# Kernel optimization log

Measured on AMD Instinct MI355X. Metric: run time of the kernel, lower is better.

## Reference

```python
import jax, jax.numpy as jnp
import numpy as np

N, E, IN, H, L = 50000, 640000, 64, 128, 3
EPS_DIST = 1e-8
LN_EPS = 1e-5


def setup_inputs() -> dict:
    key = jax.random.key(0)
    ks = iter(jax.random.split(key, 64))

    def rn(shape, fan_in):
        return (jax.random.normal(next(ks), shape, jnp.float32) / np.sqrt(fan_in)).astype(jnp.float32)

    inp = {}
    inp['h'] = jax.random.normal(next(ks), (N, IN), jnp.float32)
    inp['x'] = jax.random.normal(next(ks), (N, 3), jnp.float32)
    inp['edge_index'] = jax.random.randint(next(ks), (2, E), 0, N, jnp.int64)
    # embedding_in: Linear(IN, H)
    inp['W_emb'] = rn((IN, H), IN); inp['b_emb'] = jnp.zeros((H,), jnp.float32)
    # per-layer EquivariantConv params, stacked over L
    inp['Wm1'] = rn((L, 2 * H + 1, H), 2 * H + 1); inp['bm1'] = jnp.zeros((L, H), jnp.float32)
    inp['Wm2'] = rn((L, H, H), H);                 inp['bm2'] = jnp.zeros((L, H), jnp.float32)
    inp['Wc1'] = rn((L, H, H), H);                 inp['bc1'] = jnp.zeros((L, H), jnp.float32)
    inp['Wc2'] = rn((L, H, 1), H)  # no bias
    inp['Wn1'] = rn((L, 2 * H, H), 2 * H);         inp['bn1'] = jnp.zeros((L, H), jnp.float32)
    inp['Wn2'] = rn((L, H, H), H);                 inp['bn2'] = jnp.zeros((L, H), jnp.float32)
    inp['ln_g'] = jnp.ones((L, H), jnp.float32);   inp['ln_b'] = jnp.zeros((L, H), jnp.float32)
    # epsilon head params
    inp['Wem1'] = rn((2 * H + 4, H), 2 * H + 4);   inp['bem1'] = jnp.zeros((H,), jnp.float32)
    inp['Wem2'] = rn((H, H), H);                   inp['bem2'] = jnp.zeros((H,), jnp.float32)
    inp['Wec1'] = rn((H, H), H);                   inp['bec1'] = jnp.zeros((H,), jnp.float32)
    inp['Wec2'] = rn((H, 3), H);                   inp['bec2'] = jnp.zeros((3,), jnp.float32)
    inp['Wh1'] = rn((H + 3, H), H + 3);            inp['bh1'] = jnp.zeros((H,), jnp.float32)
    inp['Wh2'] = rn((H, 3), H);                    inp['bh2'] = jnp.zeros((3,), jnp.float32)
    return inp


def _layernorm(v, g, b):
    mu = jnp.mean(v, axis=-1, keepdims=True)
    var = jnp.mean((v - mu) ** 2, axis=-1, keepdims=True)
    return (v - mu) * jax.lax.rsqrt(var + LN_EPS) * g + b


def reference(h, x, edge_index, W_emb, b_emb, Wm1, bm1, Wm2, bm2, Wc1, bc1, Wc2,
              Wn1, bn1, Wn2, bn2, ln_g, ln_b, Wem1, bem1, Wem2, bem2,
              Wec1, bec1, Wec2, bec2, Wh1, bh1, Wh2, bh2):
    row, col = edge_index[0], edge_index[1]
    n = x.shape[0]
    seg = lambda v: jax.ops.segment_sum(v, col, num_segments=n)
    in_degree = seg(jnp.ones((col.shape[0], 1), x.dtype))  # [N,1]

    h = h @ W_emb + b_emb  # embedding_in

    for i in range(L):
        rel = x[row] - x[col]                                   # [E,3]
        dist = jnp.linalg.norm(rel, axis=-1, keepdims=True)     # [E,1]
        mi = jnp.concatenate([h[row], h[col], dist], axis=-1)   # [E,2H+1]
        m = jax.nn.silu(jax.nn.silu(mi @ Wm1[i] + bm1[i]) @ Wm2[i] + bm2[i])
        agg = seg(m)                                            # [N,H]
        rel_dir = rel / (dist + EPS_DIST)
        coord_mult = jnp.tanh(jax.nn.silu(m @ Wc1[i] + bc1[i]) @ Wc2[i])  # [E,1]
        coord_update = seg(coord_mult * rel_dir)                # [N,3]
        x = x + coord_update / (in_degree + 1.0)
        nu = jnp.concatenate([h, agg], axis=-1)
        h = h + jax.nn.silu(nu @ Wn1[i] + bn1[i]) @ Wn2[i] + bn2[i]
        h = _layernorm(h, ln_g[i], ln_b[i])

    # predict_epsilon (eps_directional_head=False, eps_use_local_head=True, eps_normalize_agg=False)
    rel = x[row] - x[col]
    dist = jnp.linalg.norm(rel, axis=-1, keepdims=True)
    mi = jnp.concatenate([h[row], h[col], rel, dist], axis=-1)  # [E,2H+4]
    em = jax.nn.silu(jax.nn.silu(mi @ Wem1 + bem1) @ Wem2 + bem2)
    eps_src = jax.nn.silu(em @ Wec1 + bec1) @ Wec2 + bec2       # [E,3]
    eps = seg(eps_src)                                          # [N,3]
    hx = jnp.concatenate([h, x], axis=-1)
    eps = eps + jax.nn.silu(hx @ Wh1 + bh1) @ Wh2 + bh2
    return (h, x, eps)
```

## Files before the change

### kernel.cpp

```cpp
#include <hip/hip_runtime.h>

#define N_NODES 50000
#define N_EDGES 640000
#define HDIM    128
#define NLAYERS 3

typedef __attribute__((ext_vector_type(4))) float f32x4;
typedef short s16x8 __attribute__((ext_vector_type(8)));
typedef __bf16 bf16v8 __attribute__((ext_vector_type(8)));

static __device__ __forceinline__ unsigned short f2b(float f){
  unsigned int u = __float_as_uint(f);
  unsigned int r = u + 0x7FFFu + ((u >> 16) & 1u);
  return (unsigned short)(r >> 16);
}
static __device__ __forceinline__ float b2f(unsigned short h){
  return __uint_as_float(((unsigned int)h) << 16);
}
static __device__ __forceinline__ float silu_f(float x){
  return x / (1.0f + __expf(-x));
}
static __device__ __forceinline__ unsigned int cvt2(float a, float b){
  unsigned int r;
  asm("v_cvt_pk_bf16_f32 %0, %1, %2" : "=v"(r) : "v"(a), "v"(b));
  return r;
}
static __device__ __forceinline__ s16x8 siluPack(const f32x4 a, const f32x4 b){
  union { unsigned int u[4]; s16x8 v; } r;
  r.u[0] = cvt2(silu_f(a[0]), silu_f(a[1]));
  r.u[1] = cvt2(silu_f(a[2]), silu_f(a[3]));
  r.u[2] = cvt2(silu_f(b[0]), silu_f(b[1]));
  r.u[3] = cvt2(silu_f(b[2]), silu_f(b[3]));
  return r.v;
}
static __device__ __forceinline__ f32x4 MFMA(s16x8 a, s16x8 b, f32x4 c){
  return __builtin_amdgcn_mfma_f32_16x16x32_bf16(
      __builtin_bit_cast(bf16v8, a), __builtin_bit_cast(bf16v8, b), c, 0, 0, 0);
}

static __device__ __forceinline__ s16x8 ldA(const unsigned short* __restrict__ WT,
                                            int K, int s, int kk, int lane){
  const unsigned short* p = WT + (size_t)((s<<4) + (lane&15))*K + (kk<<5) + ((lane>>4)<<2);
  ushort4 a = *(const ushort4*)p;
  ushort4 b = *(const ushort4*)(p + 16);
  s16x8 r;
  r[0]=(short)a.x; r[1]=(short)a.y; r[2]=(short)a.z; r[3]=(short)a.w;
  r[4]=(short)b.x; r[5]=(short)b.y; r[6]=(short)b.z; r[7]=(short)b.w;
  return r;
}
static __device__ __forceinline__ s16x8 ldBf32(const float* __restrict__ p, int q){
  float4 a = *(const float4*)(p + (q<<2));
  float4 b = *(const float4*)(p + 16 + (q<<2));
  s16x8 r;
  r[0]=(short)f2b(a.x); r[1]=(short)f2b(a.y); r[2]=(short)f2b(a.z); r[3]=(short)f2b(a.w);
  r[4]=(short)f2b(b.x); r[5]=(short)f2b(b.y); r[6]=(short)f2b(b.z); r[7]=(short)f2b(b.w);
  return r;
}

#define GLL(SRC, DST) __builtin_amdgcn_global_load_lds( \
    (const __attribute__((address_space(1))) void*)(SRC), \
    (__attribute__((address_space(3))) void*)(DST), 16, 0, 0)

struct ConvJob { const float* src; unsigned short* dst; int kshift; };
struct ConvJobs { ConvJob j[8]; };
__global__ void k_conv8(ConvJobs jobs){
  const ConvJob jb = jobs.j[blockIdx.y];
  const int K = 1 << jb.kshift;
  const int idx = (blockIdx.x<<8) + threadIdx.x;
  if (idx < (K<<7)){
    const int n = idx >> jb.kshift;
    const int k = idx & (K-1);
    jb.dst[idx] = f2b(jb.src[(size_t)k*HDIM + n]);
  }
}

struct BlobJob { const float *W1, *W2, *W3; unsigned short* dst; };
struct BlobJobs { BlobJob j[4]; };
__global__ void k_blob4(BlobJobs jobs){
  const BlobJob jb = jobs.j[blockIdx.y];
  const int i = (blockIdx.x<<8) + threadIdx.x;
  const int t = i >> 12;
  const int n = (i >> 5) & 127;
  const int slot = (i >> 3) & 3;
  const int j = i & 7;
  const int q = slot ^ ((n >> 1) & 3);
  const int kl = ((j >> 2) << 4) + (q << 2) + (j & 3);
  float v;
  if (t < 8)       v = jb.W1[(size_t)((t<<5)+kl)*HDIM + n];
  else if (t < 12) v = jb.W2[(size_t)(((t-8)<<5)+kl)*HDIM + n];
  else             v = jb.W3[(size_t)(((t-12)<<5)+kl)*HDIM + n];
  jb.dst[i] = f2b(v);
}

__global__ void k_init(const float* __restrict__ xin, float* __restrict__ xbuf,
                       float* __restrict__ cu, float* __restrict__ epsb,
                       int* __restrict__ degi){
  const int i = (blockIdx.x<<8) + threadIdx.x;
  if (i < N_NODES*3){ xbuf[i] = xin[i]; cu[i] = 0.f; epsb[i] = 0.f; }
  if (i < N_NODES) degi[i] = 0;
}

__global__ void k_degree(const int* __restrict__ coli, int* __restrict__ degi){
  const int e = (blockIdx.x<<8) + threadIdx.x;
  if (e < N_EDGES) atomicAdd(&degi[coli[e]], 1);
}
__global__ void k_scanA(const int* __restrict__ degi, int* __restrict__ off, int* __restrict__ bsum){
  const int t = threadIdx.x, b = blockIdx.x;
  const int i = (b<<8) + t;
  const int v = (i < N_NODES) ? degi[i] : 0;
  int x = v;
  const int lane = t & 63;
  #pragma unroll
  for (int d=1; d<64; d<<=1){ int y = __shfl_up(x, d); if (lane >= d) x += y; }
  __shared__ int wsum[4];
  if (lane == 63) wsum[t>>6] = x;
  __syncthreads();
  int wo = 0;
  #pragma unroll
  for (int w=0; w<4; ++w) if (w < (t>>6)) wo += wsum[w];
  const int incl = x + wo;
  if (i < N_NODES) off[i] = incl - v;
  if (t == 255) bsum[b] = incl;
}
__global__ void k_scanB(int* __restrict__ bsum, int nb){
  const int t = threadIdx.x;
  const int v = (t < nb) ? bsum[t] : 0;
  int x = v;
  const int lane = t & 63;
  #pragma unroll
  for (int d=1; d<64; d<<=1){ int y = __shfl_up(x, d); if (lane >= d) x += y; }
  __shared__ int wsum[4];
  if (lane == 63) wsum[t>>6] = x;
  __syncthreads();
  int wo = 0;
  #pragma unroll
  for (int w=0; w<4; ++w) if (w < (t>>6)) wo += wsum[w];
  const int incl = x + wo;
  if (t < nb) bsum[t] = incl - v;
}
__global__ void k_scanC(int* __restrict__ off, const int* __restrict__ bsum, int* __restrict__ cursor){
  const int i = (blockIdx.x<<8) + threadIdx.x;
  if (i < N_NODES){
    const int o = off[i] + bsum[i>>8];
    off[i] = o;
    cursor[i] = o;
  }
}
__global__ void k_fill(const int* __restrict__ coli, int* __restrict__ cursor, int* __restrict__ perm){
  const int e = (blockIdx.x<<8) + threadIdx.x;
  if (e < N_EDGES){
    const int p = atomicAdd(&cursor[coli[e]], 1);
    perm[e] = p;
  }
}

__global__ __launch_bounds__(256) void k_embed(
    const float* __restrict__ hin, const unsigned short* __restrict__ WembT,
    const float* __restrict__ bemb, float* __restrict__ hbuf,
    unsigned short* __restrict__ hb)
{
  __shared__ float s_b[128];
  const int tid = threadIdx.x;
  if (tid < 128) s_b[tid] = bemb[tid];
  __syncthreads();
  const int lane = tid & 63, q = lane>>4;
  const int n = (blockIdx.x<<6) + ((tid>>6)<<4) + (lane&15);
  const bool valid = n < N_NODES;
  const int nc = valid ? n : (N_NODES-1);
  const float* __restrict__ hp = hin + (size_t)nc*64;
  f32x4 acc[8];
  #pragma unroll
  for (int s=0;s<8;++s)
    #pragma unroll
    for (int r=0;r<4;++r) acc[s][r] = s_b[(s<<4)+(q<<2)+r];
  #pragma unroll
  for (int kk=0;kk<2;++kk){
    const s16x8 bf = ldBf32(hp + (kk<<5), q);
    #pragma unroll
    for (int s=0;s<8;++s) acc[s] = MFMA(ldA(WembT, 64, s, kk, lane), bf, acc[s]);
  }
  if (valid){
    float* op = hbuf + (size_t)n*HDIM;
    unsigned short* hbw = hb + (size_t)n*HDIM;
    #pragma unroll
    for (int s=0;s<8;++s){
      float4 o; o.x=acc[s][0]; o.y=acc[s][1]; o.z=acc[s][2]; o.w=acc[s][3];
      *(float4*)(op + (s<<4) + (q<<2)) = o;
      ushort4 u; u.x=f2b(o.x); u.y=f2b(o.y); u.z=f2b(o.z); u.w=f2b(o.w);
      *(ushort4*)(hbw + ((s>>1)<<5) + (q<<3) + ((s&1)<<2)) = u;
    }
  }
}

template<bool CSR>
__global__ __launch_bounds__(512,2) void k_edge_mlp(
    const unsigned short* __restrict__ hb, const float* __restrict__ xbuf,
    const int* __restrict__ rowi, const int* __restrict__ coli,
    const int* __restrict__ perm, const unsigned short* __restrict__ blob,
    const float* __restrict__ bm1v, const float* __restrict__ wm1r,
    const float* __restrict__ bm2v, const float* __restrict__ bc1v,
    const float* __restrict__ wc2v,
    unsigned short* __restrict__ m_buf, float* __restrict__ agg,
    float* __restrict__ cu)
{
  __shared__ struct {
    __align__(16) unsigned char wbuf[16][8192];
    int pmS[256];
    float rdS[3][256];
  } sm;
  const int tid = threadIdx.x, lane = tid & 63, q = lane >> 4;
  const int w = tid >> 6;
  const int q8 = q << 3;
  const int ebase = blockIdx.x << 8;

  #pragma unroll
  for (int t=0;t<16;++t)
    GLL(blob + (t<<12) + (tid<<3), &sm.wbuf[t][tid<<4]);

  int rn[2], cn[2];
  float dist[2];
  #pragma unroll
  for (int e=0;e<2;++e){
    const int el = (w<<5) + (e<<4) + (lane&15);
    const int ge = ebase + el;
    rn[e] = rowi[ge]; cn[e] = coli[ge];
    const float dx = xbuf[3*rn[e]+0] - xbuf[3*cn[e]+0];
    const float dy = xbuf[3*rn[e]+1] - xbuf[3*cn[e]+1];
    const float dz = xbuf[3*rn[e]+2] - xbuf[3*cn[e]+2];
    const float d = sqrtf(dx*dx + dy*dy + dz*dz);
    dist[e] = d;
    if (q == 0){
      const float inv = 1.0f / (d + 1e-8f);
      sm.rdS[0][el] = dx*inv; sm.rdS[1][el] = dy*inv; sm.rdS[2][el] = dz*inv;
      if (CSR) sm.pmS[el] = perm[ge];
    }
  }

  f32x4 acc[2][8];
  #pragma unroll
  for (int s=0;s<8;++s){
    const f32x4 b1 = *(const f32x4*)&bm1v[(s<<4)+(q<<2)];
    const f32x4 wv = *(const f32x4*)&wm1r[(s<<4)+(q<<2)];
    #pragma unroll
    for (int e=0;e<2;++e)
      #pragma unroll
      for (int r=0;r<4;++r) acc[e][s][r] = b1[r] + dist[e]*wv[r];
  }
  const int toff = ((lane&15)<<6) + ((q ^ ((lane>>1)&3))<<4);

  s16x8 B0[2], B1[2];
  #pragma unroll
  for (int e=0;e<2;++e){
    B0[e] = *(const s16x8*)(hb + ((size_t)rn[e]<<7) + q8);
    B1[e] = *(const s16x8*)(hb + ((size_t)rn[e]<<7) + 32 + q8);
  }

  __syncthreads();

  #pragma unroll
  for (int kk=0;kk<8;++kk){
    s16x8 Bn[2];
    if (kk < 6){
      const int k2 = kk+2;
      #pragma unroll
      for (int e=0;e<2;++e){
        const int node = (k2 < 4) ? rn[e] : cn[e];
        Bn[e] = *(const s16x8*)(hb + ((size_t)node<<7) + ((k2&3)<<5) + q8);
      }
    }
    #pragma unroll
    for (int s=0;s<8;++s){
      const s16x8 A = *(const s16x8*)&sm.wbuf[kk][(s<<10)+toff];
      #pragma unroll
      for (int e=0;e<2;++e) acc[e][s] = MFMA(A, B0[e], acc[e][s]);
    }
    #pragma unroll
    for (int e=0;e<2;++e){ B0[e] = B1[e]; if (kk < 6) B1[e] = Bn[e]; }
  }

  s16x8 sb[2][4];
  #pragma unroll
  for (int e=0;e<2;++e)
    #pragma unroll
    for (int c=0;c<4;++c) sb[e][c] = siluPack(acc[e][2*c], acc[e][2*c+1]);

  f32x4 acc2[2][8];
  #pragma unroll
  for (int s=0;s<8;++s){
    const f32x4 b = *(const f32x4*)&bm2v[(s<<4)+(q<<2)];
    #pragma unroll
    for (int e=0;e<2;++e) acc2[e][s] = b;
  }
  #pragma unroll
  for (int c=0;c<4;++c)
    #pragma unroll
    for (int s=0;s<8;++s){
      const s16x8 A = *(const s16x8*)&sm.wbuf[8+c][(s<<10)+toff];
      #pragma unroll
      for (int e=0;e<2;++e) acc2[e][s] = MFMA(A, sb[e][c], acc2[e][s]);
    }

  s16x8 mb[2][4];
  #pragma unroll
  for (int e=0;e<2;++e)
    #pragma unroll
    for (int c=0;c<4;++c) mb[e][c] = siluPack(acc2[e][2*c], acc2[e][2*c+1]);

  f32x4 acc3[2][8];
  #pragma unroll
  for (int s=0;s<8;++s){
    const f32x4 b = *(const f32x4*)&bc1v[(s<<4)+(q<<2)];
    #pragma unroll
    for (int e=0;e<2;++e) acc3[e][s] = b;
  }
  #pragma unroll
  for (int c=0;c<4;++c)
    #pragma unroll
    for (int s=0;s<8;++s){
      const s16x8 A = *(const s16x8*)&sm.wbuf[12+c][(s<<10)+toff];
      #pragma unroll
      for (int e=0;e<2;++e) acc3[e][s] = MFMA(A, mb[e][c], acc3[e][s]);
    }

  float dot[2] = {0.f,0.f};
  #pragma unroll
  for (int s=0;s<8;++s){
    const f32x4 wv = *(const f32x4*)&wc2v[(s<<4)+(q<<2)];
    #pragma unroll
    for (int e=0;e<2;++e)
      #pragma unroll
      for (int r=0;r<4;++r) dot[e] += silu_f(acc3[e][s][r]) * wv[r];
  }
  #pragma unroll
  for (int e=0;e<2;++e){
    dot[e] += __shfl_xor(dot[e], 16);
    dot[e] += __shfl_xor(dot[e], 32);
    const float cm = tanhf(dot[e]);
    const int el = (w<<5) + (e<<4) + (lane&15);
    if (q < 3)
      atomicAdd(&cu[(size_t)cn[e]*3 + q], cm * sm.rdS[q][el]);
  }
  if (CSR){
    #pragma unroll
    for (int e=0;e<2;++e){
      const int el = (w<<5) + (e<<4) + (lane&15);
      unsigned short* mp = m_buf + ((size_t)sm.pmS[el]<<7) + q8;
      #pragma unroll
      for (int c=0;c<4;++c) *(s16x8*)(mp + (c<<5)) = mb[e][c];
    }
  } else {
    #pragma unroll
    for (int e=0;e<2;++e){
      float* ap = agg + (size_t)cn[e]*HDIM + (q<<2);
      #pragma unroll
      for (int c=0;c<4;++c)
        #pragma unroll
        for (int j=0;j<8;++j){
          const int o = (((c<<1)+(j>>2))<<4) + (j&3);
          atomicAdd(ap + o, b2f((unsigned short)mb[e][c][j]));
        }
    }
  }
}

template<bool CSR>
__global__ __launch_bounds__(256) void k_node_mlp(
    float* __restrict__ hbuf, unsigned short* __restrict__ hb,
    float* __restrict__ xbuf,
    const unsigned short* __restrict__ m_buf, const float* __restrict__ agg,
    const int* __restrict__ off, const int* __restrict__ degi,
    float* __restrict__ cu,
    const unsigned short* __restrict__ Wn1T, const float* __restrict__ bn1v,
    const unsigned short* __restrict__ Wn2T, const float* __restrict__ bn2v,
    const float* __restrict__ lng, const float* __restrict__ lnb)
{
  __shared__ float s_bn1[128], s_bn2[128], s_g[128], s_b[128];
  const int tid = threadIdx.x;
  const int nbase = blockIdx.x << 6;
  if (tid >= 128){
    const int f = tid - 128;
    s_bn1[f]=bn1v[f]; s_bn2[f]=bn2v[f]; s_g[f]=lng[f]; s_b[f]=lnb[f];
  } else if (tid < 64){
    const int n = nbase + tid;
    if (n < N_NODES){
      const float dd = (float)degi[n] + 1.0f;
      #pragma unroll
      for (int c=0;c<3;++c){
        xbuf[3*n+c] += cu[3*n+c] / dd;
        cu[3*n+c] = 0.f;
      }
    }
  }
  __syncthreads();

  const int lane = tid & 63, q = lane >> 4;
  const int q8 = q << 3;
  const int n = nbase + ((tid>>6)<<4) + (lane & 15);
  const bool valid = (n < N_NODES);
  const int nc = valid ? n : (N_NODES-1);
  const float* __restrict__ hp = hbuf + (size_t)nc*HDIM;
  const unsigned short* __restrict__ hbp = hb + (size_t)nc*HDIM;

  float aggv[4][8];
  #pragma unroll
  for (int kk=0;kk<4;++kk)
    #pragma unroll
    for (int j=0;j<8;++j) aggv[kk][j]=0.f;
  if (CSR){
    const int st = off[nc];
    const int cnt = degi[nc];
    for (int ii=0; ii<cnt; ++ii){
      const unsigned short* mrow = m_buf + ((size_t)(st+ii)<<7);
      #pragma unroll
      for (int kk=0;kk<4;++kk){
        const s16x8 v = *(const s16x8*)(mrow + (kk<<5) + q8);
        #pragma unroll
        for (int j=0;j<8;++j) aggv[kk][j] += b2f((unsigned short)v[j]);
      }
    }
  } else {
    const float* ap = agg + (size_t)nc*HDIM;
    #pragma unroll
    for (int kk=0;kk<4;++kk){
      float4 a = *(const float4*)(ap + (kk<<5) + (q<<2));
      float4 b = *(const float4*)(ap + (kk<<5) + 16 + (q<<2));
      aggv[kk][0]=a.x; aggv[kk][1]=a.y; aggv[kk][2]=a.z; aggv[kk][3]=a.w;
      aggv[kk][4]=b.x; aggv[kk][5]=b.y; aggv[kk][6]=b.z; aggv[kk][7]=b.w;
    }
  }

  f32x4 acc[8];
  #pragma unroll
  for (int s=0;s<8;++s)
    #pragma unroll
    for (int r=0;r<4;++r) acc[s][r] = s_bn1[(s<<4)+(q<<2)+r];
  #pragma unroll
  for (int kk=0;kk<4;++kk){
    const s16x8 bf = *(const s16x8*)(hbp + (kk<<5) + q8);
    #pragma unroll
    for (int s=0;s<8;++s) acc[s] = MFMA(ldA(Wn1T, 256, s, kk, lane), bf, acc[s]);
  }
  #pragma unroll
  for (int kk=0;kk<4;++kk){
    s16x8 bf;
    #pragma unroll
    for (int j=0;j<8;++j) bf[j] = (short)f2b(aggv[kk][j]);
    #pragma unroll
    for (int s=0;s<8;++s) acc[s] = MFMA(ldA(Wn1T, 256, s, kk+4, lane), bf, acc[s]);
  }
  s16x8 sb[4];
  #pragma unroll
  for (int t=0;t<4;++t)
    #pragma unroll
    for (int j=0;j<8;++j)
      sb[t][j] = (short)f2b(silu_f(acc[(t<<1)+(j>>2)][j&3]));
  f32x4 acc2[8];
  #pragma unroll
  for (int s=0;s<8;++s)
    #pragma unroll
    for (int r=0;r<4;++r) acc2[s][r] = s_bn2[(s<<4)+(q<<2)+r];
  #pragma unroll
  for (int kk=0;kk<4;++kk){
    #pragma unroll
    for (int s=0;s<8;++s) acc2[s] = MFMA(ldA(Wn2T, 128, s, kk, lane), sb[kk], acc2[s]);
  }

  float v[8][4];
  float sum = 0.f;
  #pragma unroll
  for (int s=0;s<8;++s){
    float4 h4 = *(const float4*)(hp + (s<<4) + (q<<2));
    v[s][0] = h4.x + acc2[s][0]; v[s][1] = h4.y + acc2[s][1];
    v[s][2] = h4.z + acc2[s][2]; v[s][3] = h4.w + acc2[s][3];
    sum += v[s][0]+v[s][1]+v[s][2]+v[s][3];
  }
  sum += __shfl_xor(sum, 16);
  sum += __shfl_xor(sum, 32);
  const float mu = sum * (1.0f/128.0f);
  float vs = 0.f;
  #pragma unroll
  for (int s=0;s<8;++s)
    #pragma unroll
    for (int r=0;r<4;++r){ const float d = v[s][r]-mu; vs += d*d; }
  vs += __shfl_xor(vs, 16);
  vs += __shfl_xor(vs, 32);
  const float rs = rsqrtf(vs*(1.0f/128.0f) + 1e-5f);
  if (valid){
    float* op = hbuf + (size_t)n*HDIM;
    unsigned short* hbw = hb + (size_t)n*HDIM;
    #pragma unroll
    for (int s=0;s<8;++s){
      const int f0 = (s<<4)+(q<<2);
      float4 o;
      o.x = (v[s][0]-mu)*rs*s_g[f0+0] + s_b[f0+0];
      o.y = (v[s][1]-mu)*rs*s_g[f0+1] + s_b[f0+1];
      o.z = (v[s][2]-mu)*rs*s_g[f0+2] + s_b[f0+2];
      o.w = (v[s][3]-mu)*rs*s_g[f0+3] + s_b[f0+3];
      *(float4*)(op + f0) = o;
      ushort4 u; u.x=f2b(o.x); u.y=f2b(o.y); u.z=f2b(o.z); u.w=f2b(o.w);
      *(ushort4*)(hbw + ((s>>1)<<5) + q8 + ((s&1)<<2)) = u;
    }
  }
}

__global__ __launch_bounds__(512,2) void k_eps_edge(
    const unsigned short* __restrict__ hb, const float* __restrict__ xbuf,
    const int* __restrict__ rowi, const int* __restrict__ coli,
    const unsigned short* __restrict__ blob,
    const float* __restrict__ bem1v, const float* __restrict__ wem_rows,
    const float* __restrict__ bem2v, const float* __restrict__ bec1v,
    const float* __restrict__ Wec2, const float* __restrict__ bec2,
    float* __restrict__ epsb)
{
  __shared__ struct {
    __align__(16) unsigned char wbuf[16][8192];
    float wcs[3][128];
  } sm;
  const int tid = threadIdx.x, lane = tid & 63, q = lane >> 4;
  const int w = tid >> 6;
  const int q8 = q << 3;
  const int ebase = blockIdx.x << 8;

  #pragma unroll
  for (int t=0;t<16;++t)
    GLL(blob + (t<<12) + (tid<<3), &sm.wbuf[t][tid<<4]);
  if (tid < 128){
    sm.wcs[0][tid] = Wec2[tid*3+0];
    sm.wcs[1][tid] = Wec2[tid*3+1];
    sm.wcs[2][tid] = Wec2[tid*3+2];
  }

  int rn[2], cn[2];
  float rl0[2], rl1[2], rl2[2], dist[2];
  #pragma unroll
  for (int e=0;e<2;++e){
    const int ge = ebase + (w<<5) + (e<<4) + (lane&15);
    rn[e] = rowi[ge]; cn[e] = coli[ge];
    const float dx = xbuf[3*rn[e]+0] - xbuf[3*cn[e]+0];
    const float dy = xbuf[3*rn[e]+1] - xbuf[3*cn[e]+1];
    const float dz = xbuf[3*rn[e]+2] - xbuf[3*cn[e]+2];
    rl0[e]=dx; rl1[e]=dy; rl2[e]=dz;
    dist[e] = sqrtf(dx*dx + dy*dy + dz*dz);
  }

  f32x4 acc[2][8];
  #pragma unroll
  for (int s=0;s<8;++s){
    const int f4 = (s<<4)+(q<<2);
    const f32x4 b1 = *(const f32x4*)&bem1v[f4];
    const f32x4 w0 = *(const f32x4*)&wem_rows[f4];
    const f32x4 w1 = *(const f32x4*)&wem_rows[128+f4];
    const f32x4 w2 = *(const f32x4*)&wem_rows[256+f4];
    const f32x4 w3 = *(const f32x4*)&wem_rows[384+f4];
    #pragma unroll
    for (int e=0;e<2;++e)
      #pragma unroll
      for (int r=0;r<4;++r)
        acc[e][s][r] = b1[r] + rl0[e]*w0[r] + rl1[e]*w1[r] + rl2[e]*w2[r] + dist[e]*w3[r];
  }
  const int toff = ((lane&15)<<6) + ((q ^ ((lane>>1)&3))<<4);

  s16x8 B0[2], B1[2];
  #pragma unroll
  for (int e=0;e<2;++e){
    B0[e] = *(const s16x8*)(hb + ((size_t)rn[e]<<7) + q8);
    B1[e] = *(const s16x8*)(hb + ((size_t)rn[e]<<7) + 32 + q8);
  }

  __syncthreads();

  #pragma unroll
  for (int kk=0;kk<8;++kk){
    s16x8 Bn[2];
    if (kk < 6){
      const int k2 = kk+2;
      #pragma unroll
      for (int e=0;e<2;++e){
        const int node = (k2 < 4) ? rn[e] : cn[e];
        Bn[e] = *(const s16x8*)(hb + ((size_t)node<<7) + ((k2&3)<<5) + q8);
      }
    }
    #pragma unroll
    for (int s=0;s<8;++s){
      const s16x8 A = *(const s16x8*)&sm.wbuf[kk][(s<<10)+toff];
      #pragma unroll
      for (int e=0;e<2;++e) acc[e][s] = MFMA(A, B0[e], acc[e][s]);
    }
    #pragma unroll
    for (int e=0;e<2;++e){ B0[e] = B1[e]; if (kk < 6) B1[e] = Bn[e]; }
  }

  s16x8 sb[2][4];
  #pragma unroll
  for (int e=0;e<2;++e)
    #pragma unroll
    for (int c=0;c<4;++c) sb[e][c] = siluPack(acc[e][2*c], acc[e][2*c+1]);

  f32x4 acc2[2][8];
  #pragma unroll
  for (int s=0;s<8;++s){
    const f32x4 b = *(const f32x4*)&bem2v[(s<<4)+(q<<2)];
    #pragma unroll
    for (int e=0;e<2;++e) acc2[e][s] = b;
  }
  #pragma unroll
  for (int c=0;c<4;++c)
    #pragma unroll
    for (int s=0;s<8;++s){
      const s16x8 A = *(const s16x8*)&sm.wbuf[8+c][(s<<10)+toff];
      #pragma unroll
      for (int e=0;e<2;++e) acc2[e][s] = MFMA(A, sb[e][c], acc2[e][s]);
    }

  s16x8 mb[2][4];
  #pragma unroll
  for (int e=0;e<2;++e)
    #pragma unroll
    for (int c=0;c<4;++c) mb[e][c] = siluPack(acc2[e][2*c], acc2[e][2*c+1]);

  f32x4 acc3[2][8];
  #pragma unroll
  for (int s=0;s<8;++s){
    const f32x4 b = *(const f32x4*)&bec1v[(s<<4)+(q<<2)];
    #pragma unroll
    for (int e=0;e<2;++e) acc3[e][s] = b;
  }
  #pragma unroll
  for (int c=0;c<4;++c)
    #pragma unroll
    for (int s=0;s<8;++s){
      const s16x8 A = *(const s16x8*)&sm.wbuf[12+c][(s<<10)+toff];
      #pragma unroll
      for (int e=0;e<2;++e) acc3[e][s] = MFMA(A, mb[e][c], acc3[e][s]);
    }

  float d0[2]={0,0}, d1[2]={0,0}, d2[2]={0,0};
  #pragma unroll
  for (int s=0;s<8;++s){
    const int f4 = (s<<4)+(q<<2);
    const f32x4 w0 = *(const f32x4*)&sm.wcs[0][f4];
    const f32x4 w1 = *(const f32x4*)&sm.wcs[1][f4];
    const f32x4 w2 = *(const f32x4*)&sm.wcs[2][f4];
    #pragma unroll
    for (int e=0;e<2;++e)
      #pragma unroll
      for (int r=0;r<4;++r){
        const float ev = silu_f(acc3[e][s][r]);
        d0[e] += ev*w0[r]; d1[e] += ev*w1[r]; d2[e] += ev*w2[r];
      }
  }
  #pragma unroll
  for (int e=0;e<2;++e){
    d0[e] += __shfl_xor(d0[e],16); d0[e] += __shfl_xor(d0[e],32);
    d1[e] += __shfl_xor(d1[e],16); d1[e] += __shfl_xor(d1[e],32);
    d2[e] += __shfl_xor(d2[e],16); d2[e] += __shfl_xor(d2[e],32);
    if (q < 3){
      const float val = (q==0)?d0[e]:((q==1)?d1[e]:d2[e]);
      atomicAdd(&epsb[(size_t)cn[e]*3 + q], val + bec2[q]);
    }
  }
}

__global__ __launch_bounds__(256) void k_eps_node(
    const float* __restrict__ hbuf, const float* __restrict__ xbuf,
    const unsigned short* __restrict__ Wh1T, const float* __restrict__ bh1v,
    const float* __restrict__ wh1_rows,
    const float* __restrict__ Wh2, const float* __restrict__ bh2,
    float* __restrict__ epsb)
{
  __shared__ float s_bh1[128], s_w3[3][128], s_wc[3][128];
  const int tid = threadIdx.x;
  if (tid >= 128){
    const int f = tid - 128;
    s_bh1[f]=bh1v[f];
    s_w3[0][f]=wh1_rows[f]; s_w3[1][f]=wh1_rows[128+f]; s_w3[2][f]=wh1_rows[256+f];
    s_wc[0][f]=Wh2[f*3+0]; s_wc[1][f]=Wh2[f*3+1]; s_wc[2][f]=Wh2[f*3+2];
  }
  __syncthreads();
  const int lane = tid & 63, q = lane >> 4;
  const int n = (blockIdx.x<<6) + ((tid>>6)<<4) + (lane & 15);
  const bool valid = n < N_NODES;
  const int nc = valid ? n : (N_NODES-1);
  const float* __restrict__ hp = hbuf + (size_t)nc*HDIM;
  const float x0 = xbuf[3*nc+0], x1 = xbuf[3*nc+1], x2 = xbuf[3*nc+2];
  f32x4 acc[8];
  #pragma unroll
  for (int s=0;s<8;++s)
    #pragma unroll
    for (int r=0;r<4;++r){
      const int f = (s<<4)+(q<<2)+r;
      acc[s][r] = s_bh1[f] + x0*s_w3[0][f] + x1*s_w3[1][f] + x2*s_w3[2][f];
    }
  #pragma unroll
  for (int kk=0;kk<4;++kk){
    const s16x8 bf = ldBf32(hp + (kk<<5), q);
    #pragma unroll
    for (int s=0;s<8;++s) acc[s] = MFMA(ldA(Wh1T, 128, s, kk, lane), bf, acc[s]);
  }
  float d0=0.f, d1=0.f, d2=0.f;
  #pragma unroll
  for (int s=0;s<8;++s)
    #pragma unroll
    for (int r=0;r<4;++r){
      const int f = (s<<4)+(q<<2)+r;
      const float ev = silu_f(acc[s][r]);
      d0 += ev*s_wc[0][f]; d1 += ev*s_wc[1][f]; d2 += ev*s_wc[2][f];
    }
  d0 += __shfl_xor(d0,16); d0 += __shfl_xor(d0,32);
  d1 += __shfl_xor(d1,16); d1 += __shfl_xor(d1,32);
  d2 += __shfl_xor(d2,16); d2 += __shfl_xor(d2,32);
  if (valid && q < 3){
    const float val = (q==0)?d0:((q==1)?d1:d2);
    epsb[(size_t)n*3 + q] += val + bh2[q];
  }
}

extern "C" void kernel_launch(void* const* d_in, const int* in_sizes, int n_in,
                              void* d_out, int out_size, void* d_ws, size_t ws_size,
                              hipStream_t stream)
{
  (void)in_sizes; (void)n_in; (void)out_size;
  const float* h_in  = (const float*)d_in[0];
  const float* x_in  = (const float*)d_in[1];
  const int*   eidx  = (const int*)d_in[2];
  const float* W_emb = (const float*)d_in[3];
  const float* b_emb = (const float*)d_in[4];
  const float* Wm1 = (const float*)d_in[5];
  const float* bm1 = (const float*)d_in[6];
  const float* Wm2 = (const float*)d_in[7];
  const float* bm2 = (const float*)d_in[8];
  const float* Wc1 = (const float*)d_in[9];
  const float* bc1 = (const float*)d_in[10];
  const float* Wc2 = (const float*)d_in[11];
  const float* Wn1 = (const float*)d_in[12];
  const float* bn1 = (const float*)d_in[13];
  const float* Wn2 = (const float*)d_in[14];
  const float* bn2 = (const float*)d_in[15];
  const float* lng = (const float*)d_in[16];
  const float* lnb = (const float*)d_in[17];
  const float* Wem1 = (const float*)d_in[18];
  const float* bem1 = (const float*)d_in[19];
  const float* Wem2 = (const float*)d_in[20];
  const float* bem2 = (const float*)d_in[21];
  const float* Wec1 = (const float*)d_in[22];
  const float* bec1 = (const float*)d_in[23];
  const float* Wec2 = (const float*)d_in[24];
  const float* bec2 = (const float*)d_in[25];
  const float* Wh1 = (const float*)d_in[26];
  const float* bh1 = (const float*)d_in[27];
  const float* Wh2 = (const float*)d_in[28];
  const float* bh2 = (const float*)d_in[29];

  const int* rowi = eidx;
  const int* coli = eidx + N_EDGES;

  float* hbuf = (float*)d_out;
  float* xbuf = hbuf + (size_t)N_NODES*HDIM;
  float* epsb = xbuf + (size_t)N_NODES*3;

  char* wp = (char*)d_ws;
  auto alloc = [&](size_t bytes)->char*{
    char* p = wp; wp += (bytes + 255) & ~(size_t)255; return p;
  };
  unsigned short* WembT = (unsigned short*)alloc((size_t)128*64*2);
  unsigned short *Wn1T[NLAYERS], *Wn2T[NLAYERS];
  for (int i=0;i<NLAYERS;++i){
    Wn1T[i] = (unsigned short*)alloc((size_t)128*256*2);
    Wn2T[i] = (unsigned short*)alloc((size_t)128*128*2);
  }
  unsigned short* Wh1T  = (unsigned short*)alloc((size_t)128*128*2);
  unsigned short* blobL = (unsigned short*)alloc((size_t)NLAYERS*16*4096*2);
  unsigned short* blobE = (unsigned short*)alloc((size_t)16*4096*2);
  unsigned short* hb    = (unsigned short*)alloc((size_t)N_NODES*HDIM*2);
  int* degi   = (int*)alloc((size_t)N_NODES*4);
  int* offv   = (int*)alloc((size_t)N_NODES*4);
  int* cursor = (int*)alloc((size_t)N_NODES*4);
  int* bsum   = (int*)alloc(4096);
  float* cu   = (float*)alloc((size_t)N_NODES*3*4);
  int* perm   = (int*)alloc((size_t)N_EDGES*4);
  char* big   = alloc((size_t)N_EDGES*HDIM*2);
  const bool use_csr = ((size_t)(wp - (char*)d_ws) <= ws_size);
  unsigned short* m_buf = (unsigned short*)big;
  float* agg = (float*)big;

  ConvJobs cj;
  cj.j[0] = {W_emb, WembT, 6};
  for (int i=0;i<NLAYERS;++i){
    cj.j[1+i] = {Wn1 + (size_t)i*256*128, Wn1T[i], 8};
    cj.j[4+i] = {Wn2 + (size_t)i*128*128, Wn2T[i], 7};
  }
  cj.j[7] = {Wh1, Wh1T, 7};
  k_conv8<<<dim3(128,8), dim3(256), 0, stream>>>(cj);

  BlobJobs bj;
  for (int i=0;i<NLAYERS;++i)
    bj.j[i] = {Wm1 + (size_t)i*257*128, Wm2 + (size_t)i*128*128,
               Wc1 + (size_t)i*128*128, blobL + (size_t)i*16*4096};
  bj.j[3] = {Wem1, Wem2, Wec1, blobE};
  k_blob4<<<dim3(256,4), dim3(256), 0, stream>>>(bj);

  k_init<<<dim3((N_NODES*3+255)/256), dim3(256), 0, stream>>>(x_in, xbuf, cu, epsb, degi);

  k_degree<<<dim3((N_EDGES+255)/256), dim3(256), 0, stream>>>(coli, degi);
  const int nb = (N_NODES + 255)/256;
  if (use_csr){
    k_scanA<<<dim3(nb), dim3(256), 0, stream>>>(degi, offv, bsum);
    k_scanB<<<dim3(1), dim3(256), 0, stream>>>(bsum, nb);
    k_scanC<<<dim3(nb), dim3(256), 0, stream>>>(offv, bsum, cursor);
    k_fill<<<dim3((N_EDGES+255)/256), dim3(256), 0, stream>>>(coli, cursor, perm);
  }
  k_embed<<<dim3((N_NODES+63)/64), dim3(256), 0, stream>>>(h_in, WembT, b_emb, hbuf, hb);

  for (int i=0;i<NLAYERS;++i){
    if (!use_csr) hipMemsetAsync(agg, 0, (size_t)N_NODES*HDIM*4, stream);
    const unsigned short* blob_i = blobL + (size_t)i*16*4096;
    const float* wm1r = Wm1 + (size_t)i*257*128 + (size_t)256*128;
    if (use_csr){
      k_edge_mlp<true><<<dim3(N_EDGES/256), dim3(512), 0, stream>>>(
        hb, xbuf, rowi, coli, perm, blob_i,
        bm1 + i*128, wm1r, bm2 + i*128, bc1 + i*128, Wc2 + i*128,
        m_buf, agg, cu);
      k_node_mlp<true><<<dim3((N_NODES+63)/64), dim3(256), 0, stream>>>(
        hbuf, hb, xbuf, m_buf, agg, offv, degi, cu,
        Wn1T[i], bn1 + i*128, Wn2T[i], bn2 + i*128, lng + i*128, lnb + i*128);
    } else {
      k_edge_mlp<false><<<dim3(N_EDGES/256), dim3(512), 0, stream>>>(
        hb, xbuf, rowi, coli, perm, blob_i,
        bm1 + i*128, wm1r, bm2 + i*128, bc1 + i*128, Wc2 + i*128,
        m_buf, agg, cu);
      k_node_mlp<false><<<dim3((N_NODES+63)/64), dim3(256), 0, stream>>>(
        hbuf, hb, xbuf, m_buf, agg, offv, degi, cu,
        Wn1T[i], bn1 + i*128, Wn2T[i], bn2 + i*128, lng + i*128, lnb + i*128);
    }
  }
  k_eps_edge<<<dim3(N_EDGES/256), dim3(512), 0, stream>>>(
    hb, xbuf, rowi, coli, blobE,
    bem1, Wem1 + (size_t)256*128, bem2, bec1, Wec2, bec2, epsb);
  k_eps_node<<<dim3((N_NODES+63)/64), dim3(256), 0, stream>>>(
    hbuf, xbuf, Wh1T, bh1, Wh1 + (size_t)128*128, Wh2, bh2, epsb);
}
```

Before: 1.439 ms.

## Sort edges by destination and use segmented reductions for scatter atomics

Edges are physically reordered by destination node during CSR fill, so the edge kernels process sorted (row, col) arrays and write messages contiguously instead of through a permutation. The coordinate and epsilon scatters now do a 16-lane segmented reduction over equal keys, so only one atomic is issued per run of edges sharing a destination. Edge kernels move to 1024-thread blocks covering 512 edges, which spreads the shared-weight load across more threads. The non-CSR fallback is removed, so the workspace must always be large enough for the message buffer.

```diff
diff --git a/kernel.cpp b/kernel.cpp
--- a/kernel.cpp
+++ b/kernel.cpp
@@ -60,6 +60,19 @@
 #define GLL(SRC, DST) __builtin_amdgcn_global_load_lds( \
     (const __attribute__((address_space(1))) void*)(SRC), \
     (__attribute__((address_space(3))) void*)(DST), 16, 0, 0)
+
+static __device__ __forceinline__ void segAtomicAdd(float* addr_base, int key,
+                                                    float v, int lane, int q){
+  #pragma unroll
+  for (int d=1; d<16; d<<=1){
+    const float ov = __shfl_up(v, d);
+    const int  ok = __shfl_up(key, d);
+    if ((lane&15) >= d && ok == key) v += ov;
+  }
+  const int nk = __shfl_down(key, 1);
+  const bool last = ((lane&15)==15) || (nk != key);
+  if (last) atomicAdd(addr_base + (size_t)key*3 + q, v);
+}
 
 struct ConvJob { const float* src; unsigned short* dst; int kshift; };
 struct ConvJobs { ConvJob j[8]; };
@@ -146,11 +159,15 @@
     cursor[i] = o;
   }
 }
-__global__ void k_fill(const int* __restrict__ coli, int* __restrict__ cursor, int* __restrict__ perm){
+__global__ void k_fill(const int* __restrict__ rowi, const int* __restrict__ coli,
+                       int* __restrict__ cursor,
+                       int* __restrict__ rowS, int* __restrict__ colS){
   const int e = (blockIdx.x<<8) + threadIdx.x;
   if (e < N_EDGES){
-    const int p = atomicAdd(&cursor[coli[e]], 1);
-    perm[e] = p;
+    const int c = coli[e];
+    const int p = atomicAdd(&cursor[c], 1);
+    rowS[p] = rowi[e];
+    colS[p] = c;
   }
 }
 
@@ -192,30 +209,31 @@
   }
 }
 
-template<bool CSR>
-__global__ __launch_bounds__(512,2) void k_edge_mlp(
+__global__ __launch_bounds__(1024,1) void k_edge_mlp(
     const unsigned short* __restrict__ hb, const float* __restrict__ xbuf,
-    const int* __restrict__ rowi, const int* __restrict__ coli,
-    const int* __restrict__ perm, const unsigned short* __restrict__ blob,
+    const int* __restrict__ rowS, const int* __restrict__ colS,
+    const unsigned short* __restrict__ blob,
     const float* __restrict__ bm1v, const float* __restrict__ wm1r,
     const float* __restrict__ bm2v, const float* __restrict__ bc1v,
     const float* __restrict__ wc2v,
-    unsigned short* __restrict__ m_buf, float* __restrict__ agg,
-    float* __restrict__ cu)
+    unsigned short* __restrict__ m_buf, float* __restrict__ cu)
 {
   __shared__ struct {
     __align__(16) unsigned char wbuf[16][8192];
-    int pmS[256];
-    float rdS[3][256];
+    float rdS[3][512];
   } sm;
   const int tid = threadIdx.x, lane = tid & 63, q = lane >> 4;
   const int w = tid >> 6;
   const int q8 = q << 3;
-  const int ebase = blockIdx.x << 8;
-
-  #pragma unroll
-  for (int t=0;t<16;++t)
-    GLL(blob + (t<<12) + (tid<<3), &sm.wbuf[t][tid<<4]);
+  const int ebase = blockIdx.x << 9;
+
+  {
+    const unsigned short* bsrc = blob + (tid<<3);
+    unsigned char* bdst = ((unsigned char*)sm.wbuf) + (tid<<4);
+    #pragma unroll
+    for (int i=0;i<8;++i)
+      GLL(bsrc + (i<<13), bdst + (i<<14));
+  }
 
   int rn[2], cn[2];
   float dist[2];
@@ -223,7 +241,7 @@
   for (int e=0;e<2;++e){
     const int el = (w<<5) + (e<<4) + (lane&15);
     const int ge = ebase + el;
-    rn[e] = rowi[ge]; cn[e] = coli[ge];
+    rn[e] = rowS[ge]; cn[e] = colS[ge];
     const float dx = xbuf[3*rn[e]+0] - xbuf[3*cn[e]+0];
     const float dy = xbuf[3*rn[e]+1] - xbuf[3*cn[e]+1];
     const float dz = xbuf[3*rn[e]+2] - xbuf[3*cn[e]+2];
@@ -232,7 +250,6 @@
     if (q == 0){
       const float inv = 1.0f / (d + 1e-8f);
       sm.rdS[0][el] = dx*inv; sm.rdS[1][el] = dy*inv; sm.rdS[2][el] = dz*inv;
-      if (CSR) sm.pmS[el] = perm[ge];
     }
   }
 
@@ -338,36 +355,21 @@
     const float cm = tanhf(dot[e]);
     const int el = (w<<5) + (e<<4) + (lane&15);
     if (q < 3)
-      atomicAdd(&cu[(size_t)cn[e]*3 + q], cm * sm.rdS[q][el]);
-  }
-  if (CSR){
-    #pragma unroll
-    for (int e=0;e<2;++e){
-      const int el = (w<<5) + (e<<4) + (lane&15);
-      unsigned short* mp = m_buf + ((size_t)sm.pmS[el]<<7) + q8;
-      #pragma unroll
-      for (int c=0;c<4;++c) *(s16x8*)(mp + (c<<5)) = mb[e][c];
-    }
-  } else {
-    #pragma unroll
-    for (int e=0;e<2;++e){
-      float* ap = agg + (size_t)cn[e]*HDIM + (q<<2);
-      #pragma unroll
-      for (int c=0;c<4;++c)
-        #pragma unroll
-        for (int j=0;j<8;++j){
-          const int o = (((c<<1)+(j>>2))<<4) + (j&3);
-          atomicAdd(ap + o, b2f((unsigned short)mb[e][c][j]));
-        }
-    }
-  }
-}
-
-template<bool CSR>
+      segAtomicAdd(cu, cn[e], cm * sm.rdS[q][el], lane, q);
+  }
+  #pragma unroll
+  for (int e=0;e<2;++e){
+    const int ge = ebase + (w<<5) + (e<<4) + (lane&15);
+    unsigned short* mp = m_buf + ((size_t)ge<<7) + q8;
+    #pragma unroll
+    for (int c=0;c<4;++c) *(s16x8*)(mp + (c<<5)) = mb[e][c];
+  }
+}
+
 __global__ __launch_bounds__(256) void k_node_mlp(
     float* __restrict__ hbuf, unsigned short* __restrict__ hb,
     float* __restrict__ xbuf,
-    const unsigned short* __restrict__ m_buf, const float* __restrict__ agg,
+    const unsigned short* __restrict__ m_buf,
     const int* __restrict__ off, const int* __restrict__ degi,
     float* __restrict__ cu,
     const unsigned short* __restrict__ Wn1T, const float* __restrict__ bn1v,
@@ -406,7 +408,7 @@
   for (int kk=0;kk<4;++kk)
     #pragma unroll
     for (int j=0;j<8;++j) aggv[kk][j]=0.f;
-  if (CSR){
+  {
     const int st = off[nc];
     const int cnt = degi[nc];
     for (int ii=0; ii<cnt; ++ii){
@@ -417,15 +419,6 @@
         #pragma unroll
         for (int j=0;j<8;++j) aggv[kk][j] += b2f((unsigned short)v[j]);
       }
-    }
-  } else {
-    const float* ap = agg + (size_t)nc*HDIM;
-    #pragma unroll
-    for (int kk=0;kk<4;++kk){
-      float4 a = *(const float4*)(ap + (kk<<5) + (q<<2));
-      float4 b = *(const float4*)(ap + (kk<<5) + 16 + (q<<2));
-      aggv[kk][0]=a.x; aggv[kk][1]=a.y; aggv[kk][2]=a.z; aggv[kk][3]=a.w;
-      aggv[kk][4]=b.x; aggv[kk][5]=b.y; aggv[kk][6]=b.z; aggv[kk][7]=b.w;
     }
   }
 
@@ -503,9 +496,9 @@
   }
 }
 
-__global__ __launch_bounds__(512,2) void k_eps_edge(
+__global__ __launch_bounds__(1024,1) void k_eps_edge(
     const unsigned short* __restrict__ hb, const float* __restrict__ xbuf,
-    const int* __restrict__ rowi, const int* __restrict__ coli,
+    const int* __restrict__ rowS, const int* __restrict__ colS,
     const unsigned short* __restrict__ blob,
     const float* __restrict__ bem1v, const float* __restrict__ wem_rows,
     const float* __restrict__ bem2v, const float* __restrict__ bec1v,
@@ -519,11 +512,15 @@
   const int tid = threadIdx.x, lane = tid & 63, q = lane >> 4;
   const int w = tid >> 6;
   const int q8 = q << 3;
-  const int ebase = blockIdx.x << 8;
-
-  #pragma unroll
-  for (int t=0;t<16;++t)
-    GLL(blob + (t<<12) + (tid<<3), &sm.wbuf[t][tid<<4]);
+  const int ebase = blockIdx.x << 9;
+
+  {
+    const unsigned short* bsrc = blob + (tid<<3);
+    unsigned char* bdst = ((unsigned char*)sm.wbuf) + (tid<<4);
+    #pragma unroll
+    for (int i=0;i<8;++i)
+      GLL(bsrc + (i<<13), bdst + (i<<14));
+  }
   if (tid < 128){
     sm.wcs[0][tid] = Wec2[tid*3+0];
     sm.wcs[1][tid] = Wec2[tid*3+1];
@@ -535,7 +532,7 @@
   #pragma unroll
   for (int e=0;e<2;++e){
     const int ge = ebase + (w<<5) + (e<<4) + (lane&15);
-    rn[e] = rowi[ge]; cn[e] = coli[ge];
+    rn[e] = rowS[ge]; cn[e] = colS[ge];
     const float dx = xbuf[3*rn[e]+0] - xbuf[3*cn[e]+0];
     const float dy = xbuf[3*rn[e]+1] - xbuf[3*cn[e]+1];
     const float dz = xbuf[3*rn[e]+2] - xbuf[3*cn[e]+2];
@@ -655,8 +652,8 @@
     d1[e] += __shfl_xor(d1[e],16); d1[e] += __shfl_xor(d1[e],32);
     d2[e] += __shfl_xor(d2[e],16); d2[e] += __shfl_xor(d2[e],32);
     if (q < 3){
-      const float val = (q==0)?d0[e]:((q==1)?d1[e]:d2[e]);
-      atomicAdd(&epsb[(size_t)cn[e]*3 + q], val + bec2[q]);
+      const float val = ((q==0)?d0[e]:((q==1)?d1[e]:d2[e])) + bec2[q];
+      segAtomicAdd(epsb, cn[e], val, lane, q);
     }
   }
 }
@@ -719,7 +716,7 @@
                               void* d_out, int out_size, void* d_ws, size_t ws_size,
                               hipStream_t stream)
 {
-  (void)in_sizes; (void)n_in; (void)out_size;
+  (void)in_sizes; (void)n_in; (void)out_size; (void)ws_size;
   const float* h_in  = (const float*)d_in[0];
   const float* x_in  = (const float*)d_in[1];
   const int*   eidx  = (const int*)d_in[2];
@@ -777,11 +774,9 @@
   int* cursor = (int*)alloc((size_t)N_NODES*4);
   int* bsum   = (int*)alloc(4096);
   float* cu   = (float*)alloc((size_t)N_NODES*3*4);
-  int* perm   = (int*)alloc((size_t)N_EDGES*4);
-  char* big   = alloc((size_t)N_EDGES*HDIM*2);
-  const bool use_csr = ((size_t)(wp - (char*)d_ws) <= ws_size);
-  unsigned short* m_buf = (unsigned short*)big;
-  float* agg = (float*)big;
+  int* rowS   = (int*)alloc((size_t)N_EDGES*4);
+  int* colS   = (int*)alloc((size_t)N_EDGES*4);
+  unsigned short* m_buf = (unsigned short*)alloc((size_t)N_EDGES*HDIM*2);
 
   ConvJobs cj;
   cj.j[0] = {W_emb, WembT, 6};
@@ -803,38 +798,26 @@
 
   k_degree<<<dim3((N_EDGES+255)/256), dim3(256), 0, stream>>>(coli, degi);
   const int nb = (N_NODES + 255)/256;
-  if (use_csr){
-    k_scanA<<<dim3(nb), dim3(256), 0, stream>>>(degi, offv, bsum);
-    k_scanB<<<dim3(1), dim3(256), 0, stream>>>(bsum, nb);
-    k_scanC<<<dim3(nb), dim3(256), 0, stream>>>(offv, bsum, cursor);
-    k_fill<<<dim3((N_EDGES+255)/256), dim3(256), 0, stream>>>(coli, cursor, perm);
-  }
+  k_scanA<<<dim3(nb), dim3(256), 0, stream>>>(degi, offv, bsum);
+  k_scanB<<<dim3(1), dim3(256), 0, stream>>>(bsum, nb);
+  k_scanC<<<dim3(nb), dim3(256), 0, stream>>>(offv, bsum, cursor);
+  k_fill<<<dim3((N_EDGES+255)/256), dim3(256), 0, stream>>>(rowi, coli, cursor, rowS, colS);
+
   k_embed<<<dim3((N_NODES+63)/64), dim3(256), 0, stream>>>(h_in, WembT, b_emb, hbuf, hb);
 
   for (int i=0;i<NLAYERS;++i){
-    if (!use_csr) hipMemsetAsync(agg, 0, (size_t)N_NODES*HDIM*4, stream);
     const unsigned short* blob_i = blobL + (size_t)i*16*4096;
     const float* wm1r = Wm1 + (size_t)i*257*128 + (size_t)256*128;
-    if (use_csr){
-      k_edge_mlp<true><<<dim3(N_EDGES/256), dim3(512), 0, stream>>>(
-        hb, xbuf, rowi, coli, perm, blob_i,
-        bm1 + i*128, wm1r, bm2 + i*128, bc1 + i*128, Wc2 + i*128,
-        m_buf, agg, cu);
-      k_node_mlp<true><<<dim3((N_NODES+63)/64), dim3(256), 0, stream>>>(
-        hbuf, hb, xbuf, m_buf, agg, offv, degi, cu,
-        Wn1T[i], bn1 + i*128, Wn2T[i], bn2 + i*128, lng + i*128, lnb + i*128);
-    } else {
-      k_edge_mlp<false><<<dim3(N_EDGES/256), dim3(512), 0, stream>>>(
-        hb, xbuf, rowi, coli, perm, blob_i,
-        bm1 + i*128, wm1r, bm2 + i*128, bc1 + i*128, Wc2 + i*128,
-        m_buf, agg, cu);
-      k_node_mlp<false><<<dim3((N_NODES+63)/64), dim3(256), 0, stream>>>(
-        hbuf, hb, xbuf, m_buf, agg, offv, degi, cu,
-        Wn1T[i], bn1 + i*128, Wn2T[i], bn2 + i*128, lng + i*128, lnb + i*128);
-    }
-  }
-  k_eps_edge<<<dim3(N_EDGES/256), dim3(512), 0, stream>>>(
-    hb, xbuf, rowi, coli, blobE,
+    k_edge_mlp<<<dim3(N_EDGES/512), dim3(1024), 0, stream>>>(
+      hb, xbuf, rowS, colS, blob_i,
+      bm1 + i*128, wm1r, bm2 + i*128, bc1 + i*128, Wc2 + i*128,
+      m_buf, cu);
+    k_node_mlp<<<dim3((N_NODES+63)/64), dim3(256), 0, stream>>>(
+      hbuf, hb, xbuf, m_buf, offv, degi, cu,
+      Wn1T[i], bn1 + i*128, Wn2T[i], bn2 + i*128, lng + i*128, lnb + i*128);
+  }
+  k_eps_edge<<<dim3(N_EDGES/512), dim3(1024), 0, stream>>>(
+    hb, xbuf, rowS, colS, blobE,
     bem1, Wem1 + (size_t)256*128, bem2, bec1, Wec2, bec2, epsb);
   k_eps_node<<<dim3((N_NODES+63)/64), dim3(256), 0, stream>>>(
     hbuf, xbuf, Wh1T, bh1, Wh1 + (size_t)128*128, Wh2, bh2, epsb);
```

Measured after the change: 1.373 ms. 4.5% less time.
